# Optimization experiments

Measured on AMD Instinct MI355X. Metric: run time of the kernel, lower is better.

Reference implementation:

```python
import jax, jax.numpy as jnp
import numpy as np

D_MODEL = 1024
N_HEADS = 16
N_KV = 8
GROUP = N_HEADS // N_KV  # 2
D_HEAD = D_MODEL // N_HEADS  # 64
SCALE = D_HEAD ** -0.5


def setup_inputs() -> dict:
    key = jax.random.key(0)
    ks = jax.random.split(key, 5)
    s = 0.02
    return {
        "x": jax.random.normal(ks[0], (2, 2048, D_MODEL), dtype=jnp.float32),
        "Wq": jax.random.normal(ks[1], (D_MODEL, D_MODEL), dtype=jnp.float32) * s,
        "Wk": jax.random.normal(ks[2], (N_KV * D_HEAD, D_MODEL), dtype=jnp.float32) * s,
        "Wv": jax.random.normal(ks[3], (N_KV * D_HEAD, D_MODEL), dtype=jnp.float32) * s,
        "Wproj": jax.random.normal(ks[4], (D_MODEL, D_MODEL), dtype=jnp.float32) * s,
    }


def reference(x, Wq, Wk, Wv, Wproj):
    b, t, c = x.shape
    # projections (torch Linear: x @ W.T)
    q = (x @ Wq.T).reshape(b, t, N_KV, GROUP, D_HEAD)  # heads ordered (kv, group)
    k = (x @ Wk.T).reshape(b, t, N_KV, D_HEAD)
    v = (x @ Wv.T).reshape(b, t, N_KV, D_HEAD)
    # repeat_interleave(K/V, group, dim=heads) == broadcast over the group axis,
    # since q head index h maps to kv head h // GROUP.
    scores = jnp.einsum('btkgd,bskd->bkgts', q, k) * SCALE  # (b, kv, g, t, s)
    attn = jax.nn.softmax(scores, axis=-1)
    y = jnp.einsum('bkgts,bskd->btkgd', attn, v)  # (b, t, kv, g, d)
    y = y.reshape(b, t, c)
    return y @ Wproj.T
```

## Files before the change

### kernel.cpp

```cpp
#include <hip/hip_runtime.h>


#define SEQ    2048
#define CDIM   1024
#define KVDIM  512
#define SCL2E  0.18033688011112042f

typedef __attribute__((ext_vector_type(8))) short   bf16x8;
typedef __attribute__((ext_vector_type(4))) float   f32x4;
typedef unsigned short ushort_t;

__device__ __forceinline__ ushort_t f2bf(float f) {
    unsigned u = __float_as_uint(f);
    u += 0x7FFFu + ((u >> 16) & 1u);
    return (ushort_t)(u >> 16);
}
__device__ __forceinline__ float bf2f(ushort_t h) {
    return __uint_as_float(((unsigned)h) << 16);
}
__device__ __forceinline__ void load_lds16(const void* g, void* l) {
    __builtin_amdgcn_global_load_lds(
        (const __attribute__((address_space(1))) void*)g,
        (__attribute__((address_space(3))) void*)l, 16, 0, 0);
}

__global__ __launch_bounds__(256) void cvt_bf16(
    const float* __restrict__ x,  const float* __restrict__ wq,
    const float* __restrict__ wk, const float* __restrict__ wv,
    const float* __restrict__ wp,
    ushort_t* __restrict__ xh,  ushort_t* __restrict__ wqh,
    ushort_t* __restrict__ wkh, ushort_t* __restrict__ wvh,
    ushort_t* __restrict__ wph)
{
    const int i = blockIdx.x * 256 + threadIdx.x;
    const float* src; ushort_t* dst; int off;
    if (i < 1048576)      { src = x;  dst = xh;  off = i; }
    else if (i < 1310720) { src = wq; dst = wqh; off = i - 1048576; }
    else if (i < 1441792) { src = wk; dst = wkh; off = i - 1310720; }
    else if (i < 1572864) { src = wv; dst = wvh; off = i - 1441792; }
    else                  { src = wp; dst = wph; off = i - 1572864; }
    const float4 v = ((const float4*)src)[off];
    ushort4 h;
    h.x = f2bf(v.x); h.y = f2bf(v.y); h.z = f2bf(v.z); h.w = f2bf(v.w);
    ((ushort4*)dst)[off] = h;
}

__global__ __launch_bounds__(256, 4) void gemm64(
    const ushort_t* __restrict__ A, int K,
    const ushort_t* __restrict__ B1, void* __restrict__ C1, int N1, int epi1, float sc1,
    const ushort_t* __restrict__ B2, void* __restrict__ C2, int N2, int epi2, float sc2,
    const ushort_t* __restrict__ B3, void* __restrict__ C3, int N3, int epi3, float sc3)
{
    __shared__ ushort_t sA[128 * 64];
    __shared__ ushort_t sB[64 * 64];

    const int tid = threadIdx.x, wv = tid >> 6, lane = tid & 63;
    const int lm = lane & 15, quad = lane >> 4;

    const int gdx = gridDim.x;
    const int nwg = gdx * gridDim.y;
    int id = blockIdx.y * gdx + blockIdx.x;
    id = (id & 7) * (nwg >> 3) + (id >> 3);
    const int bx = id % gdx;
    const int m0 = (id / gdx) * 128;

    const int t1 = N1 >> 6, t2 = N2 >> 6;
    const ushort_t* B; void* Cv; int n0, Nout, epi; float sc;
    if (bx < t1)           { B = B1; Cv = C1; Nout = N1; epi = epi1; sc = sc1; n0 = bx * 64; }
    else if (bx < t1 + t2) { B = B2; Cv = C2; Nout = N2; epi = epi2; sc = sc2; n0 = (bx - t1) * 64; }
    else                   { B = B3; Cv = C3; Nout = N3; epi = epi3; sc = sc3; n0 = (bx - t1 - t2) * 64; }

    const int mh = wv >> 1, nh = wv & 1;
    const int srow = lane >> 3;
    const int scol = ((lane & 7) ^ ((lane >> 3) & 7)) * 8;

    f32x4 acc[4][2] = {};

    for (int k0 = 0; k0 < K; k0 += 64) {
        __syncthreads();
        #pragma unroll
        for (int i = 0; i < 6; ++i) {
            const int g = wv * 6 + i;
            if (g < 16)
                load_lds16(A + (size_t)(m0 + g * 8 + srow) * K + k0 + scol, sA + g * 512);
            else
                load_lds16(B + (size_t)(n0 + (g - 16) * 8 + srow) * K + k0 + scol, sB + (g - 16) * 512);
        }
        __syncthreads();

        #pragma unroll
        for (int ks = 0; ks < 2; ++ks) {
            const int co = ((ks * 4 + quad) ^ (lm & 7)) * 8;
            bf16x8 a[4], b[2];
            #pragma unroll
            for (int mt = 0; mt < 4; ++mt)
                a[mt] = *(const bf16x8*)&sA[(mh * 64 + mt * 16 + lm) * 64 + co];
            #pragma unroll
            for (int nt = 0; nt < 2; ++nt)
                b[nt] = *(const bf16x8*)&sB[(nh * 32 + nt * 16 + lm) * 64 + co];
            #pragma unroll
            for (int mt = 0; mt < 4; ++mt)
                #pragma unroll
                for (int nt = 0; nt < 2; ++nt)
                    acc[mt][nt] = __builtin_amdgcn_mfma_f32_16x16x32_bf16(a[mt], b[nt], acc[mt][nt], 0, 0, 0);
        }
    }

    if (epi == 0) {
        float* C = (float*)Cv;
        #pragma unroll
        for (int mt = 0; mt < 4; ++mt)
            #pragma unroll
            for (int nt = 0; nt < 2; ++nt)
                #pragma unroll
                for (int r = 0; r < 4; ++r)
                    C[(size_t)(m0 + mh * 64 + mt * 16 + quad * 4 + r) * Nout + n0 + nh * 32 + nt * 16 + lm]
                        = acc[mt][nt][r];
    } else if (epi == 2) {
        ushort_t* C = (ushort_t*)Cv;
        const int bB   = m0 >> 11;
        const int tloc = (m0 & 2047) + mh * 64 + quad * 4;
        #pragma unroll
        for (int mt = 0; mt < 4; ++mt)
            #pragma unroll
            for (int nt = 0; nt < 2; ++nt) {
                const int n = n0 + nh * 32 + nt * 16 + lm;
                ushort4 u;
                u.x = f2bf(acc[mt][nt][0]);
                u.y = f2bf(acc[mt][nt][1]);
                u.z = f2bf(acc[mt][nt][2]);
                u.w = f2bf(acc[mt][nt][3]);
                *(ushort4*)&C[(size_t)(bB * KVDIM + n) * SEQ + tloc + mt * 16] = u;
            }
    } else {
        ushort_t* C = (ushort_t*)Cv;
        #pragma unroll
        for (int mt = 0; mt < 4; ++mt)
            #pragma unroll
            for (int nt = 0; nt < 2; ++nt)
                #pragma unroll
                for (int r = 0; r < 4; ++r)
                    C[(size_t)(m0 + mh * 64 + mt * 16 + quad * 4 + r) * Nout + n0 + nh * 32 + nt * 16 + lm]
                        = f2bf(acc[mt][nt][r] * sc);
    }
}

__global__ __launch_bounds__(128, 1) void attn5(
    const ushort_t* __restrict__ Qh, const ushort_t* __restrict__ Kh,
    const ushort_t* __restrict__ Vth, ushort_t* __restrict__ Yh)
{
    __shared__ ushort_t sK[2][64 * 64];
    __shared__ ushort_t sV[2][64 * 64];

    const int tid = threadIdx.x, wv = tid >> 6, lane = tid & 63;
    const int lm = lane & 15, quad = lane >> 4;
    const int b = blockIdx.y >> 4, h = blockIdx.y & 15, kvh = h >> 1;
    const int t0 = blockIdx.x * 128, tq0 = t0 + wv * 64;

    bf16x8 qh[4][2];
    #pragma unroll
    for (int qg = 0; qg < 4; ++qg) {
        const size_t rb = (size_t)(b * SEQ + tq0 + qg * 16 + lm) * CDIM + h * 64;
        #pragma unroll
        for (int ks = 0; ks < 2; ++ks)
            qh[qg][ks] = *(const bf16x8*)(Qh + rb + ks * 32 + quad * 8);
    }

    const ushort_t* gK = Kh  + (size_t)b * SEQ * KVDIM + kvh * 64;
    const ushort_t* gV = Vth + (size_t)(b * 8 + kvh) * 64 * SEQ;

    const int srow = lane >> 3;
    const int scol = ((lane & 7) ^ ((lane >> 3) & 7)) * 8;

    int krow[8];
    #pragma unroll
    for (int it = 0; it < 8; ++it) {
        const int lr = it * 8 + srow;
        krow[it] = (lr & 0x20) | ((lr & 0x10) >> 2) | ((lr & 0x0C) << 1) | (lr & 3);
    }

    float l_r[4] = {0.0f, 0.0f, 0.0f, 0.0f};
    f32x4 O[4][4] = {};

    if (wv == 0) {
        #pragma unroll
        for (int it = 0; it < 8; ++it)
            load_lds16(gK + (size_t)krow[it] * KVDIM + scol, &sK[0][it * 512]);
    } else {
        #pragma unroll
        for (int it = 0; it < 8; ++it)
            load_lds16(gV + (size_t)(it * 8 + srow) * SEQ + scol, &sV[0][it * 512]);
    }

    typedef union { bf16x8 v; unsigned u[4]; } pku;

    for (int kt = 0; kt < SEQ / 64; ++kt) {
        const int cur = kt & 1;
        __syncthreads();

        if (kt + 1 < SEQ / 64) {
            const int s1 = (kt + 1) * 64;
            if (wv == 0) {
                #pragma unroll
                for (int it = 0; it < 8; ++it)
                    load_lds16(gK + (size_t)(s1 + krow[it]) * KVDIM + scol,
                               &sK[cur ^ 1][it * 512]);
            } else {
                #pragma unroll
                for (int it = 0; it < 8; ++it)
                    load_lds16(gV + (size_t)(it * 8 + srow) * SEQ + s1 + scol,
                               &sV[cur ^ 1][it * 512]);
            }
        }

        f32x4 st[4][4] = {};
        __builtin_amdgcn_s_setprio(1);
        #pragma unroll
        for (int sti = 0; sti < 4; ++sti)
            #pragma unroll
            for (int ks = 0; ks < 2; ++ks) {
                const int off = (sti * 16 + lm) * 64 + (((ks * 4 + quad) ^ (lm & 7)) * 8);
                const bf16x8 kf = *(const bf16x8*)&sK[cur][off];
                #pragma unroll
                for (int qg = 0; qg < 4; ++qg)
                    st[qg][sti] = __builtin_amdgcn_mfma_f32_16x16x32_bf16(kf, qh[qg][ks], st[qg][sti], 0, 0, 0);
            }
        __builtin_amdgcn_s_setprio(0);

        pku pa[4][2];
        #pragma unroll
        for (int qg = 0; qg < 4; ++qg)
            #pragma unroll
            for (int sti = 0; sti < 4; ++sti) {
                const float p0 = __builtin_amdgcn_exp2f(st[qg][sti][0]);
                const float p1 = __builtin_amdgcn_exp2f(st[qg][sti][1]);
                const float p2 = __builtin_amdgcn_exp2f(st[qg][sti][2]);
                const float p3 = __builtin_amdgcn_exp2f(st[qg][sti][3]);
                l_r[qg] += (p0 + p1) + (p2 + p3);
                pa[qg][sti >> 1].u[(sti & 1) * 2 + 0] =
                    __builtin_amdgcn_perm(__float_as_uint(p1), __float_as_uint(p0), 0x07060302u);
                pa[qg][sti >> 1].u[(sti & 1) * 2 + 1] =
                    __builtin_amdgcn_perm(__float_as_uint(p3), __float_as_uint(p2), 0x07060302u);
            }

        __builtin_amdgcn_s_setprio(1);
        #pragma unroll
        for (int ks = 0; ks < 2; ++ks) {
            const int co = ((ks * 4 + quad) ^ (lm & 7)) * 8;
            #pragma unroll
            for (int dt = 0; dt < 4; ++dt) {
                const bf16x8 vt = *(const bf16x8*)&sV[cur][(dt * 16 + lm) * 64 + co];
                #pragma unroll
                for (int qg = 0; qg < 4; ++qg)
                    O[qg][dt] = __builtin_amdgcn_mfma_f32_16x16x32_bf16(pa[qg][ks].v, vt, O[qg][dt], 0, 0, 0);
            }
        }
        __builtin_amdgcn_s_setprio(0);
    }

    #pragma unroll
    for (int qg = 0; qg < 4; ++qg) {
        l_r[qg] += __shfl_xor(l_r[qg], 16);
        l_r[qg] += __shfl_xor(l_r[qg], 32);
    }
    #pragma unroll
    for (int qg = 0; qg < 4; ++qg)
        #pragma unroll
        for (int r = 0; r < 4; ++r) {
            const float lq = __shfl(l_r[qg], (lane & 48) | (quad * 4 + r));
            const float inv = 1.0f / lq;
            const int t = tq0 + qg * 16 + quad * 4 + r;
            const size_t rowb = (size_t)(b * SEQ + t) * CDIM + h * 64;
            #pragma unroll
            for (int dt = 0; dt < 4; ++dt)
                Yh[rowb + dt * 16 + lm] = f2bf(O[qg][dt][r] * inv);
        }
}

extern "C" void kernel_launch(void* const* d_in, const int* in_sizes, int n_in,
                              void* d_out, int out_size, void* d_ws, size_t ws_size,
                              hipStream_t stream)
{
    const float* x     = (const float*)d_in[0];
    const float* Wq    = (const float*)d_in[1];
    const float* Wk    = (const float*)d_in[2];
    const float* Wv    = (const float*)d_in[3];
    const float* Wproj = (const float*)d_in[4];
    float* out = (float*)d_out;

    const int M = 2 * SEQ;

    char* p = (char*)d_ws;
    ushort_t* xh   = (ushort_t*)p; p += (size_t)M * CDIM * 2;
    ushort_t* wqh  = (ushort_t*)p; p += (size_t)CDIM * CDIM * 2;
    ushort_t* wkh  = (ushort_t*)p; p += (size_t)KVDIM * CDIM * 2;
    ushort_t* wvh  = (ushort_t*)p; p += (size_t)KVDIM * CDIM * 2;
    ushort_t* wph  = (ushort_t*)p; p += (size_t)CDIM * CDIM * 2;
    ushort_t* qh   = (ushort_t*)p; p += (size_t)M * CDIM * 2;
    ushort_t* kh   = (ushort_t*)p; p += (size_t)M * KVDIM * 2;
    ushort_t* vth  = (ushort_t*)p; p += (size_t)M * KVDIM * 2;
    ushort_t* yh = xh;

    dim3 blk(256);

    cvt_bf16<<<dim3(7168), blk, 0, stream>>>(
        x, Wq, Wk, Wv, Wproj, xh, wqh, wkh, wvh, wph);

    gemm64<<<dim3(32, 32), blk, 0, stream>>>(
        xh, CDIM,
        wqh, qh,  CDIM,  3, SCL2E,
        wkh, kh,  KVDIM, 3, 1.0f,
        wvh, vth, KVDIM, 2, 1.0f);

    attn5<<<dim3(SEQ / 128, 32), dim3(128), 0, stream>>>(qh, kh, vth, yh);

    gemm64<<<dim3(16, 32), blk, 0, stream>>>(
        yh, CDIM,
        wph, out, CDIM, 0, 1.0f,
        nullptr, nullptr, 0, 0, 1.0f,
        nullptr, nullptr, 0, 0, 1.0f);
}
```

Before: 168.2 us.

## Restructure attention kernel to 4 waves of 16 query rows each

```diff
diff --git a/kernel.cpp b/kernel.cpp
--- a/kernel.cpp
+++ b/kernel.cpp
@@ -145,7 +145,7 @@
     }
 }
 
-__global__ __launch_bounds__(128, 1) void attn5(
+__global__ __launch_bounds__(256, 4) void attn6(
     const ushort_t* __restrict__ Qh, const ushort_t* __restrict__ Kh,
     const ushort_t* __restrict__ Vth, ushort_t* __restrict__ Yh)
 {
@@ -155,41 +155,41 @@
     const int tid = threadIdx.x, wv = tid >> 6, lane = tid & 63;
     const int lm = lane & 15, quad = lane >> 4;
     const int b = blockIdx.y >> 4, h = blockIdx.y & 15, kvh = h >> 1;
-    const int t0 = blockIdx.x * 128, tq0 = t0 + wv * 64;
-
-    bf16x8 qh[4][2];
-    #pragma unroll
-    for (int qg = 0; qg < 4; ++qg) {
-        const size_t rb = (size_t)(b * SEQ + tq0 + qg * 16 + lm) * CDIM + h * 64;
+    const int t0 = blockIdx.x * 64, tq0 = t0 + wv * 16;
+
+    bf16x8 qh[2];
+    {
+        const size_t rb = (size_t)(b * SEQ + tq0 + lm) * CDIM + h * 64;
         #pragma unroll
         for (int ks = 0; ks < 2; ++ks)
-            qh[qg][ks] = *(const bf16x8*)(Qh + rb + ks * 32 + quad * 8);
+            qh[ks] = *(const bf16x8*)(Qh + rb + ks * 32 + quad * 8);
     }
 
     const ushort_t* gK = Kh  + (size_t)b * SEQ * KVDIM + kvh * 64;
     const ushort_t* gV = Vth + (size_t)(b * 8 + kvh) * 64 * SEQ;
 
+    const int g0 = (wv & 1) * 4;
     const int srow = lane >> 3;
     const int scol = ((lane & 7) ^ ((lane >> 3) & 7)) * 8;
 
-    int krow[8];
+    int krow[4];
     #pragma unroll
-    for (int it = 0; it < 8; ++it) {
-        const int lr = it * 8 + srow;
+    for (int it = 0; it < 4; ++it) {
+        const int lr = (g0 + it) * 8 + srow;
         krow[it] = (lr & 0x20) | ((lr & 0x10) >> 2) | ((lr & 0x0C) << 1) | (lr & 3);
     }
 
-    float l_r[4] = {0.0f, 0.0f, 0.0f, 0.0f};
-    f32x4 O[4][4] = {};
-
-    if (wv == 0) {
-        #pragma unroll
-        for (int it = 0; it < 8; ++it)
-            load_lds16(gK + (size_t)krow[it] * KVDIM + scol, &sK[0][it * 512]);
+    float l_r = 0.0f;
+    f32x4 O[4] = {};
+
+    if (wv < 2) {
+        #pragma unroll
+        for (int it = 0; it < 4; ++it)
+            load_lds16(gK + (size_t)krow[it] * KVDIM + scol, &sK[0][(g0 + it) * 512]);
     } else {
         #pragma unroll
-        for (int it = 0; it < 8; ++it)
-            load_lds16(gV + (size_t)(it * 8 + srow) * SEQ + scol, &sV[0][it * 512]);
+        for (int it = 0; it < 4; ++it)
+            load_lds16(gV + (size_t)((g0 + it) * 8 + srow) * SEQ + scol, &sV[0][(g0 + it) * 512]);
     }
 
     typedef union { bf16x8 v; unsigned u[4]; } pku;
@@ -200,20 +200,20 @@
 
         if (kt + 1 < SEQ / 64) {
             const int s1 = (kt + 1) * 64;
-            if (wv == 0) {
-                #pragma unroll
-                for (int it = 0; it < 8; ++it)
+            if (wv < 2) {
+                #pragma unroll
+                for (int it = 0; it < 4; ++it)
                     load_lds16(gK + (size_t)(s1 + krow[it]) * KVDIM + scol,
-                               &sK[cur ^ 1][it * 512]);
+                               &sK[cur ^ 1][(g0 + it) * 512]);
             } else {
                 #pragma unroll
-                for (int it = 0; it < 8; ++it)
-                    load_lds16(gV + (size_t)(it * 8 + srow) * SEQ + s1 + scol,
-                               &sV[cur ^ 1][it * 512]);
+                for (int it = 0; it < 4; ++it)
+                    load_lds16(gV + (size_t)((g0 + it) * 8 + srow) * SEQ + s1 + scol,
+                               &sV[cur ^ 1][(g0 + it) * 512]);
             }
         }
 
-        f32x4 st[4][4] = {};
+        f32x4 st[4] = {};
         __builtin_amdgcn_s_setprio(1);
         #pragma unroll
         for (int sti = 0; sti < 4; ++sti)
@@ -221,27 +221,23 @@
             for (int ks = 0; ks < 2; ++ks) {
                 const int off = (sti * 16 + lm) * 64 + (((ks * 4 + quad) ^ (lm & 7)) * 8);
                 const bf16x8 kf = *(const bf16x8*)&sK[cur][off];
-                #pragma unroll
-                for (int qg = 0; qg < 4; ++qg)
-                    st[qg][sti] = __builtin_amdgcn_mfma_f32_16x16x32_bf16(kf, qh[qg][ks], st[qg][sti], 0, 0, 0);
+                st[sti] = __builtin_amdgcn_mfma_f32_16x16x32_bf16(kf, qh[ks], st[sti], 0, 0, 0);
             }
         __builtin_amdgcn_s_setprio(0);
 
-        pku pa[4][2];
-        #pragma unroll
-        for (int qg = 0; qg < 4; ++qg)
-            #pragma unroll
-            for (int sti = 0; sti < 4; ++sti) {
-                const float p0 = __builtin_amdgcn_exp2f(st[qg][sti][0]);
-                const float p1 = __builtin_amdgcn_exp2f(st[qg][sti][1]);
-                const float p2 = __builtin_amdgcn_exp2f(st[qg][sti][2]);
-                const float p3 = __builtin_amdgcn_exp2f(st[qg][sti][3]);
-                l_r[qg] += (p0 + p1) + (p2 + p3);
-                pa[qg][sti >> 1].u[(sti & 1) * 2 + 0] =
-                    __builtin_amdgcn_perm(__float_as_uint(p1), __float_as_uint(p0), 0x07060302u);
-                pa[qg][sti >> 1].u[(sti & 1) * 2 + 1] =
-                    __builtin_amdgcn_perm(__float_as_uint(p3), __float_as_uint(p2), 0x07060302u);
-            }
+        pku pa[2];
+        #pragma unroll
+        for (int sti = 0; sti < 4; ++sti) {
+            const float p0 = __builtin_amdgcn_exp2f(st[sti][0]);
+            const float p1 = __builtin_amdgcn_exp2f(st[sti][1]);
+            const float p2 = __builtin_amdgcn_exp2f(st[sti][2]);
+            const float p3 = __builtin_amdgcn_exp2f(st[sti][3]);
+            l_r += (p0 + p1) + (p2 + p3);
+            pa[sti >> 1].u[(sti & 1) * 2 + 0] =
+                __builtin_amdgcn_perm(__float_as_uint(p1), __float_as_uint(p0), 0x07060302u);
+            pa[sti >> 1].u[(sti & 1) * 2 + 1] =
+                __builtin_amdgcn_perm(__float_as_uint(p3), __float_as_uint(p2), 0x07060302u);
+        }
 
         __builtin_amdgcn_s_setprio(1);
         #pragma unroll
@@ -250,31 +246,24 @@
             #pragma unroll
             for (int dt = 0; dt < 4; ++dt) {
                 const bf16x8 vt = *(const bf16x8*)&sV[cur][(dt * 16 + lm) * 64 + co];
-                #pragma unroll
-                for (int qg = 0; qg < 4; ++qg)
-                    O[qg][dt] = __builtin_amdgcn_mfma_f32_16x16x32_bf16(pa[qg][ks].v, vt, O[qg][dt], 0, 0, 0);
+                O[dt] = __builtin_amdgcn_mfma_f32_16x16x32_bf16(pa[ks].v, vt, O[dt], 0, 0, 0);
             }
         }
         __builtin_amdgcn_s_setprio(0);
     }
 
+    l_r += __shfl_xor(l_r, 16);
+    l_r += __shfl_xor(l_r, 32);
     #pragma unroll
-    for (int qg = 0; qg < 4; ++qg) {
-        l_r[qg] += __shfl_xor(l_r[qg], 16);
-        l_r[qg] += __shfl_xor(l_r[qg], 32);
-    }
-    #pragma unroll
-    for (int qg = 0; qg < 4; ++qg)
-        #pragma unroll
-        for (int r = 0; r < 4; ++r) {
-            const float lq = __shfl(l_r[qg], (lane & 48) | (quad * 4 + r));
-            const float inv = 1.0f / lq;
-            const int t = tq0 + qg * 16 + quad * 4 + r;
-            const size_t rowb = (size_t)(b * SEQ + t) * CDIM + h * 64;
-            #pragma unroll
-            for (int dt = 0; dt < 4; ++dt)
-                Yh[rowb + dt * 16 + lm] = f2bf(O[qg][dt][r] * inv);
-        }
+    for (int r = 0; r < 4; ++r) {
+        const float lq = __shfl(l_r, (lane & 48) | (quad * 4 + r));
+        const float inv = 1.0f / lq;
+        const int t = tq0 + quad * 4 + r;
+        const size_t rowb = (size_t)(b * SEQ + t) * CDIM + h * 64;
+        #pragma unroll
+        for (int dt = 0; dt < 4; ++dt)
+            Yh[rowb + dt * 16 + lm] = f2bf(O[dt][r] * inv);
+    }
 }
 
 extern "C" void kernel_launch(void* const* d_in, const int* in_sizes, int n_in,
@@ -312,7 +301,7 @@
         wkh, kh,  KVDIM, 3, 1.0f,
         wvh, vth, KVDIM, 2, 1.0f);
 
-    attn5<<<dim3(SEQ / 128, 32), dim3(128), 0, stream>>>(qh, kh, vth, yh);
+    attn6<<<dim3(SEQ / 64, 32), blk, 0, stream>>>(qh, kh, vth, yh);
 
     gemm64<<<dim3(16, 32), blk, 0, stream>>>(
         yh, CDIM,
```

New measurement: 169.9 us. About the same (+1.0%).
